# Kernel optimization log

Hardware: AMD Instinct MI355X
Metric: run time of the kernel (lower is better)

## Reference

```python
import jax, jax.numpy as jnp
import numpy as np

C = 4096  # d_model (RWKV-7B scale)


def setup_inputs() -> dict:
    key = jax.random.key(0)
    ks = jax.random.split(key, 14)
    vec = lambda k: jax.random.normal(k, (C,), dtype=jnp.float32)
    mat = lambda k: jax.random.normal(k, (C, C), dtype=jnp.float32) * 0.02
    return {
        "x": vec(ks[0]),
        "state": vec(ks[1]),
        "state_a": vec(ks[2]),
        # state_b is a running sum of exponentials in RWKV -> strictly positive
        "state_b": jax.random.uniform(ks[3], (C,), dtype=jnp.float32) + 0.5,
        "state_p": vec(ks[4]),
        "time_mix_k": jax.random.uniform(ks[5], (C,), dtype=jnp.float32),
        "time_mix_v": jax.random.uniform(ks[6], (C,), dtype=jnp.float32),
        "time_mix_r": jax.random.uniform(ks[7], (C,), dtype=jnp.float32),
        "time_first": vec(ks[8]) * 0.5,
        # time_decay is negative in RWKV (exp decay of the state)
        "time_decay": -jnp.abs(vec(ks[9])) - 0.1,
        "kw": mat(ks[10]),
        "vw": mat(ks[11]),
        "rw": mat(ks[12]),
        "ow": mat(ks[13]),
    }


def reference(x, state, state_a, state_b, state_p,
              time_mix_k, time_mix_v, time_mix_r,
              time_first, time_decay, kw, vw, rw, ow):
    # token-shift interpolation with previous token (state)
    xk = x * time_mix_k + state * (1.0 - time_mix_k)
    xv = x * time_mix_v + state * (1.0 - time_mix_v)
    xr = x * time_mix_r + state * (1.0 - time_mix_r)
    new_state = x

    r = jax.nn.sigmoid(rw @ xr)   # [C]
    kk = kw @ xk                  # [C]
    vv = vw @ xv                  # [C]

    aa, bb, pp = state_a, state_b, state_p

    # output accumulators with max-trick stabilization
    ww = time_first + kk
    p = jnp.maximum(pp, ww)
    e1 = jnp.exp(pp - p)
    e2 = jnp.exp(ww - p)
    a = e1 * aa + e2 * vv
    b = e1 * bb + e2

    # state update (decayed accumulators)
    ww = pp + time_decay
    p = jnp.maximum(ww, kk)
    e1 = jnp.exp(ww - p)
    e2 = jnp.exp(kk - p)
    new_state_a = e1 * aa + e2 * vv
    new_state_b = e1 * bb + e2
    new_state_p = p

    wkv = a / b
    out = ow @ (r * wkv)
    return (out, new_state, new_state_a, new_state_b, new_state_p)
```

## Files before the change

kernel.cpp:

```cpp
#include <hip/hip_runtime.h>
#include <math.h>

#define C 4096

typedef float f4 __attribute__((ext_vector_type(4)));

__global__ __launch_bounds__(256, 6) void matvec3_kernel(
    const float* __restrict__ kw, const float* __restrict__ vw, const float* __restrict__ rw,
    const float* __restrict__ x, const float* __restrict__ state,
    const float* __restrict__ tmk, const float* __restrict__ tmv, const float* __restrict__ tmr,
    float* __restrict__ kk, float* __restrict__ vvo, float* __restrict__ rr) {
    __shared__ f4 xs[C / 4];

    const int t = threadIdx.x;
    const int m = blockIdx.x >> 9;

    const float* W;
    const float* tm;
    float* out;
    if (m == 0)      { W = kw; tm = tmk; out = kk;  }
    else if (m == 1) { W = vw; tm = tmv; out = vvo; }
    else             { W = rw; tm = tmr; out = rr;  }

    const f4* x4 = (const f4*)x;
    const f4* s4 = (const f4*)state;
    const f4* t4 = (const f4*)tm;
#pragma unroll
    for (int j = 0; j < 4; ++j) {
        int i = j * 256 + t;
        f4 xi = x4[i], si = s4[i], ti = t4[i];
        f4 r;
        r.x = xi.x * ti.x + si.x * (1.0f - ti.x);
        r.y = xi.y * ti.y + si.y * (1.0f - ti.y);
        r.z = xi.z * ti.z + si.z * (1.0f - ti.z);
        r.w = xi.w * ti.w + si.w * (1.0f - ti.w);
        xs[i] = r;
    }
    __syncthreads();

    const int wave = t >> 6;
    const int lane = t & 63;
    const int r0 = (blockIdx.x & 511) * 8 + wave * 2;
    const int r1 = r0 + 1;
    const f4* W0 = (const f4*)(W + (size_t)r0 * C);
    const f4* W1 = (const f4*)(W + (size_t)r1 * C);

    f4 acc0 = {0.f, 0.f, 0.f, 0.f};
    f4 acc1 = {0.f, 0.f, 0.f, 0.f};
#pragma unroll
    for (int it = 0; it < 16; ++it) {
        f4 w0 = W0[it * 64 + lane];
        f4 w1 = W1[it * 64 + lane];
        f4 xx = xs[it * 64 + lane];
        acc0.x += w0.x * xx.x; acc0.y += w0.y * xx.y;
        acc0.z += w0.z * xx.z; acc0.w += w0.w * xx.w;
        acc1.x += w1.x * xx.x; acc1.y += w1.y * xx.y;
        acc1.z += w1.z * xx.z; acc1.w += w1.w * xx.w;
    }
    float sum0 = (acc0.x + acc0.y) + (acc0.z + acc0.w);
    float sum1 = (acc1.x + acc1.y) + (acc1.z + acc1.w);
#pragma unroll
    for (int off = 32; off > 0; off >>= 1) {
        sum0 += __shfl_down(sum0, off, 64);
        sum1 += __shfl_down(sum1, off, 64);
    }
    if (lane == 0) { out[r0] = sum0; out[r1] = sum1; }
}

__global__ void wkv_kernel(const float* __restrict__ kk, const float* __restrict__ vv,
                           const float* __restrict__ rr,
                           const float* __restrict__ aa, const float* __restrict__ bb,
                           const float* __restrict__ pp,
                           const float* __restrict__ time_first,
                           const float* __restrict__ time_decay,
                           const float* __restrict__ x,
                           float* __restrict__ rwkv,
                           float* __restrict__ new_state,
                           float* __restrict__ out_sa, float* __restrict__ out_sb,
                           float* __restrict__ out_sp) {
    int i = blockIdx.x * blockDim.x + threadIdx.x;
    if (i < C) {
        float k = kk[i], v = vv[i];
        float a_ = aa[i], b_ = bb[i], p_ = pp[i];

        float ww = time_first[i] + k;
        float p  = fmaxf(p_, ww);
        float e1 = expf(p_ - p);
        float e2 = expf(ww - p);
        float a  = e1 * a_ + e2 * v;
        float b  = e1 * b_ + e2;

        float ww2 = p_ + time_decay[i];
        float p2  = fmaxf(ww2, k);
        float e1b = expf(ww2 - p2);
        float e2b = expf(k - p2);
        out_sa[i] = e1b * a_ + e2b * v;
        out_sb[i] = e1b * b_ + e2b;
        out_sp[i] = p2;

        new_state[i] = x[i];

        float r = 1.0f / (1.0f + expf(-rr[i]));
        rwkv[i] = r * (a / b);
    }
}

__global__ __launch_bounds__(256, 6) void matvec_kernel(const float* __restrict__ W,
                                                        const float* __restrict__ xin,
                                                        float* __restrict__ out) {
    __shared__ f4 xs[C / 4];
    const int t = threadIdx.x;

    const f4* x4 = (const f4*)xin;
#pragma unroll
    for (int j = 0; j < 4; ++j) {
        int i = j * 256 + t;
        xs[i] = x4[i];
    }
    __syncthreads();

    const int wave = t >> 6;
    const int lane = t & 63;
    const int r0 = blockIdx.x * 8 + wave * 2;
    const int r1 = r0 + 1;
    const f4* W0 = (const f4*)(W + (size_t)r0 * C);
    const f4* W1 = (const f4*)(W + (size_t)r1 * C);

    f4 acc0 = {0.f, 0.f, 0.f, 0.f};
    f4 acc1 = {0.f, 0.f, 0.f, 0.f};
#pragma unroll
    for (int it = 0; it < 16; ++it) {
        f4 w0 = W0[it * 64 + lane];
        f4 w1 = W1[it * 64 + lane];
        f4 xx = xs[it * 64 + lane];
        acc0.x += w0.x * xx.x; acc0.y += w0.y * xx.y;
        acc0.z += w0.z * xx.z; acc0.w += w0.w * xx.w;
        acc1.x += w1.x * xx.x; acc1.y += w1.y * xx.y;
        acc1.z += w1.z * xx.z; acc1.w += w1.w * xx.w;
    }
    float sum0 = (acc0.x + acc0.y) + (acc0.z + acc0.w);
    float sum1 = (acc1.x + acc1.y) + (acc1.z + acc1.w);
#pragma unroll
    for (int off = 32; off > 0; off >>= 1) {
        sum0 += __shfl_down(sum0, off, 64);
        sum1 += __shfl_down(sum1, off, 64);
    }
    if (lane == 0) { out[r0] = sum0; out[r1] = sum1; }
}

extern "C" void kernel_launch(void* const* d_in, const int* in_sizes, int n_in,
                              void* d_out, int out_size, void* d_ws, size_t ws_size,
                              hipStream_t stream) {
    const float* x          = (const float*)d_in[0];
    const float* state      = (const float*)d_in[1];
    const float* state_a    = (const float*)d_in[2];
    const float* state_b    = (const float*)d_in[3];
    const float* state_p    = (const float*)d_in[4];
    const float* tmk        = (const float*)d_in[5];
    const float* tmv        = (const float*)d_in[6];
    const float* tmr        = (const float*)d_in[7];
    const float* time_first = (const float*)d_in[8];
    const float* time_decay = (const float*)d_in[9];
    const float* kw         = (const float*)d_in[10];
    const float* vw         = (const float*)d_in[11];
    const float* rw         = (const float*)d_in[12];
    const float* ow         = (const float*)d_in[13];

    float* out       = (float*)d_out;
    float* new_state = out + C;
    float* new_sa    = out + 2 * C;
    float* new_sb    = out + 3 * C;
    float* new_sp    = out + 4 * C;

    float* ws   = (float*)d_ws;
    float* kk   = ws;
    float* vv   = ws + C;
    float* rr   = ws + 2 * C;
    float* rwkv = ws + 3 * C;

    matvec3_kernel<<<3 * C / 8, 256, 0, stream>>>(kw, vw, rw, x, state, tmk, tmv, tmr,
                                                  kk, vv, rr);

    wkv_kernel<<<C / 256, 256, 0, stream>>>(kk, vv, rr, state_a, state_b, state_p,
                                            time_first, time_decay, x,
                                            rwkv, new_state, new_sa, new_sb, new_sp);

    matvec_kernel<<<C / 8, 256, 0, stream>>>(ow, rwkv, out);
}
```

Baseline: 259.4 us.

## Fuse WKV elementwise step into output matvec, recomputing per block

```diff
diff --git a/kernel.cpp b/kernel.cpp
--- a/kernel.cpp
+++ b/kernel.cpp
@@ -67,85 +67,96 @@
     if (lane == 0) { out[r0] = sum0; out[r1] = sum1; }
 }
 
-__global__ void wkv_kernel(const float* __restrict__ kk, const float* __restrict__ vv,
-                           const float* __restrict__ rr,
-                           const float* __restrict__ aa, const float* __restrict__ bb,
-                           const float* __restrict__ pp,
-                           const float* __restrict__ time_first,
-                           const float* __restrict__ time_decay,
-                           const float* __restrict__ x,
-                           float* __restrict__ rwkv,
-                           float* __restrict__ new_state,
-                           float* __restrict__ out_sa, float* __restrict__ out_sb,
-                           float* __restrict__ out_sp) {
-    int i = blockIdx.x * blockDim.x + threadIdx.x;
-    if (i < C) {
-        float k = kk[i], v = vv[i];
-        float a_ = aa[i], b_ = bb[i], p_ = pp[i];
-
-        float ww = time_first[i] + k;
-        float p  = fmaxf(p_, ww);
-        float e1 = expf(p_ - p);
-        float e2 = expf(ww - p);
-        float a  = e1 * a_ + e2 * v;
-        float b  = e1 * b_ + e2;
-
-        float ww2 = p_ + time_decay[i];
-        float p2  = fmaxf(ww2, k);
-        float e1b = expf(ww2 - p2);
-        float e2b = expf(k - p2);
-        out_sa[i] = e1b * a_ + e2b * v;
-        out_sb[i] = e1b * b_ + e2b;
-        out_sp[i] = p2;
-
-        new_state[i] = x[i];
-
-        float r = 1.0f / (1.0f + expf(-rr[i]));
-        rwkv[i] = r * (a / b);
-    }
-}
-
-__global__ __launch_bounds__(256, 6) void matvec_kernel(const float* __restrict__ W,
-                                                        const float* __restrict__ xin,
-                                                        float* __restrict__ out) {
+__global__ __launch_bounds__(256) void wkv_matvec_kernel(
+    const float* __restrict__ W,
+    const float* __restrict__ kk, const float* __restrict__ vv, const float* __restrict__ rr,
+    const float* __restrict__ aa, const float* __restrict__ bb, const float* __restrict__ pp,
+    const float* __restrict__ time_first, const float* __restrict__ time_decay,
+    const float* __restrict__ x,
+    float* __restrict__ out, float* __restrict__ new_state,
+    float* __restrict__ out_sa, float* __restrict__ out_sb, float* __restrict__ out_sp) {
     __shared__ f4 xs[C / 4];
     const int t = threadIdx.x;
+    const bool writer = (blockIdx.x == 0);
 
-    const f4* x4 = (const f4*)xin;
+    const f4* kk4 = (const f4*)kk;
+    const f4* vv4 = (const f4*)vv;
+    const f4* rr4 = (const f4*)rr;
+    const f4* aa4 = (const f4*)aa;
+    const f4* bb4 = (const f4*)bb;
+    const f4* pp4 = (const f4*)pp;
+    const f4* tf4 = (const f4*)time_first;
+    const f4* td4 = (const f4*)time_decay;
+    const f4* x4  = (const f4*)x;
+    f4* sa4 = (f4*)out_sa;
+    f4* sb4 = (f4*)out_sb;
+    f4* sp4 = (f4*)out_sp;
+    f4* ns4 = (f4*)new_state;
+
 #pragma unroll
     for (int j = 0; j < 4; ++j) {
         int i = j * 256 + t;
-        xs[i] = x4[i];
+        f4 kf = kk4[i], vf = vv4[i], rf = rr4[i];
+        f4 af = aa4[i], bf = bb4[i], pf = pp4[i];
+        f4 tff = tf4[i], tdf = td4[i];
+        f4 rwkv, sa, sb, sp;
+
+#define WKV1(cc)                                                             \
+        {                                                                    \
+            float k = kf.cc, v = vf.cc;                                      \
+            float A = af.cc, B = bf.cc, P = pf.cc;                           \
+            float ww = tff.cc + k;                                           \
+            float p  = fmaxf(P, ww);                                         \
+            float e1 = expf(P - p);                                          \
+            float e2 = expf(ww - p);                                         \
+            float a  = e1 * A + e2 * v;                                      \
+            float b  = e1 * B + e2;                                          \
+            float ww2 = P + tdf.cc;                                          \
+            float p2  = fmaxf(ww2, k);                                       \
+            float e1b = expf(ww2 - p2);                                      \
+            float e2b = expf(k - p2);                                        \
+            sa.cc = e1b * A + e2b * v;                                       \
+            sb.cc = e1b * B + e2b;                                           \
+            sp.cc = p2;                                                      \
+            float r = 1.0f / (1.0f + expf(-rf.cc));                          \
+            rwkv.cc = r * (a / b);                                           \
+        }
+        WKV1(x) WKV1(y) WKV1(z) WKV1(w)
+#undef WKV1
+
+        xs[i] = rwkv;
+        if (writer) {
+            sa4[i] = sa;
+            sb4[i] = sb;
+            sp4[i] = sp;
+            ns4[i] = x4[i];
+        }
     }
     __syncthreads();
 
     const int wave = t >> 6;
     const int lane = t & 63;
-    const int r0 = blockIdx.x * 8 + wave * 2;
-    const int r1 = r0 + 1;
-    const f4* W0 = (const f4*)(W + (size_t)r0 * C);
-    const f4* W1 = (const f4*)(W + (size_t)r1 * C);
+    const int row  = blockIdx.x * 4 + wave;
+    const f4* Wrow = (const f4*)(W + (size_t)row * C);
 
-    f4 acc0 = {0.f, 0.f, 0.f, 0.f};
-    f4 acc1 = {0.f, 0.f, 0.f, 0.f};
+    f4 wreg[16];
+#pragma unroll
+    for (int it = 0; it < 16; ++it) wreg[it] = Wrow[it * 64 + lane];
+
+    float s0 = 0.f, s1 = 0.f, s2 = 0.f, s3 = 0.f;
 #pragma unroll
     for (int it = 0; it < 16; ++it) {
-        f4 w0 = W0[it * 64 + lane];
-        f4 w1 = W1[it * 64 + lane];
         f4 xx = xs[it * 64 + lane];
-        acc0.x += w0.x * xx.x; acc0.y += w0.y * xx.y;
-        acc0.z += w0.z * xx.z; acc0.w += w0.w * xx.w;
-        acc1.x += w1.x * xx.x; acc1.y += w1.y * xx.y;
-        acc1.z += w1.z * xx.z; acc1.w += w1.w * xx.w;
+        f4 w  = wreg[it];
+        s0 += w.x * xx.x;
+        s1 += w.y * xx.y;
+        s2 += w.z * xx.z;
+        s3 += w.w * xx.w;
     }
-    float sum0 = (acc0.x + acc0.y) + (acc0.z + acc0.w);
-    float sum1 = (acc1.x + acc1.y) + (acc1.z + acc1.w);
+    float sum = (s0 + s1) + (s2 + s3);
 #pragma unroll
-    for (int off = 32; off > 0; off >>= 1) {
-        sum0 += __shfl_down(sum0, off, 64);
-        sum1 += __shfl_down(sum1, off, 64);
-    }
-    if (lane == 0) { out[r0] = sum0; out[r1] = sum1; }
+    for (int off = 32; off > 0; off >>= 1) sum += __shfl_down(sum, off, 64);
+    if (lane == 0) out[row] = sum;
 }
 
 extern "C" void kernel_launch(void* const* d_in, const int* in_sizes, int n_in,
@@ -172,18 +183,16 @@
     float* new_sb    = out + 3 * C;
     float* new_sp    = out + 4 * C;
 
-    float* ws   = (float*)d_ws;
-    float* kk   = ws;
-    float* vv   = ws + C;
-    float* rr   = ws + 2 * C;
-    float* rwkv = ws + 3 * C;
+    float* ws = (float*)d_ws;
+    float* kk = ws;
+    float* vv = ws + C;
+    float* rr = ws + 2 * C;
 
     matvec3_kernel<<<3 * C / 8, 256, 0, stream>>>(kw, vw, rw, x, state, tmk, tmv, tmr,
                                                   kk, vv, rr);
 
-    wkv_kernel<<<C / 256, 256, 0, stream>>>(kk, vv, rr, state_a, state_b, state_p,
-                                            time_first, time_decay, x,
-                                            rwkv, new_state, new_sa, new_sb, new_sp);
-
-    matvec_kernel<<<C / 8, 256, 0, stream>>>(ow, rwkv, out);
+    wkv_matvec_kernel<<<C / 4, 256, 0, stream>>>(ow, kk, vv, rr,
+                                                 state_a, state_b, state_p,
+                                                 time_first, time_decay, x,
+                                                 out, new_state, new_sa, new_sb, new_sp);
 }
```

Result: no change. 259.4 us (median of 2 runs) (-0.0%).
